# Kernel optimization log

Measured on AMD Instinct MI355X. Metric: run time of the kernel, lower is better.

## Reference

```python
import jax, jax.numpy as jnp
import numpy as np


def hadamard_matrix(n):
    # Sylvester construction; n must be a power of 2.
    H = np.array([[1.0]], dtype=np.float32)
    while H.shape[0] < n:
        H = np.block([[H, H], [H, -H]])
    return H


def setup_inputs() -> dict:
    key = jax.random.key(0)
    k1, k2, k3 = jax.random.split(key, 3)
    B, C, Hh, Ww, P = 8, 64, 256, 256, 4
    x = jax.random.normal(k1, (B, C, Hh, Ww), dtype=jnp.float32)
    v = jax.random.uniform(k2, (P, Hh, Ww), dtype=jnp.float32)          # torch.rand init
    T = jax.random.uniform(k3, (P, Hh, Ww), dtype=jnp.float32) / 10.0   # torch.rand/10 init
    return {"x": x, "v": v, "T": T}


def _wht2d(u, Hm, sc):
    # normalized Walsh-Hadamard transform along last two axes (H symmetric)
    u = jnp.einsum('...hw,vw->...hv', u, Hm) * sc   # axis=-1
    u = jnp.einsum('...hv,gh->...gv', u, Hm) * sc   # axis=-2
    return u


def reference(x, v, T):
    n = x.shape[-1]  # 256, power of 2; height_pad==height so no padding
    Hm = jnp.asarray(hadamard_matrix(n), dtype=x.dtype)
    sc = jnp.asarray(1.0 / np.sqrt(n), dtype=x.dtype)
    f2 = _wht2d(x, Hm, sc)                              # (B,C,H,W)
    a = f2[None] * v[:, None, None]                     # (P,B,C,H,W)
    st = jnp.tanh(a) * jax.nn.relu(jnp.abs(a) - jnp.abs(T)[:, None, None])
    f6 = st.sum(axis=0)                                 # (B,C,H,W)
    f8 = _wht2d(f6, Hm, sc)
    return f8 + x                                       # residual=True
```

## Files before the change

kernel.cpp:

```cpp
#include <hip/hip_runtime.h>
#include <hip/hip_fp16.h>


#define NPX 65536
#define SC  0.0625f

__device__ __forceinline__ unsigned int h2u(__half2 h) {
  union { __half2 h; unsigned int u; } c; c.h = h; return c.u;
}
__device__ __forceinline__ __half2 u2h(unsigned int u) {
  union { __half2 h; unsigned int u; } c; c.u = u; return c.h;
}

__device__ __forceinline__ void fwht16(float f[16]) {
  #pragma unroll
  for (int d = 1; d < 16; d <<= 1) {
    #pragma unroll
    for (int i = 0; i < 16; ++i) {
      if (!(i & d)) {
        float a = f[i], b = f[i | d];
        f[i]     = a + b;
        f[i | d] = a - b;
      }
    }
  }
}

__device__ __forceinline__ void fwht256_wave(float r[4], int lane) {
  float a0 = r[0] + r[1], b0 = r[0] - r[1];
  float a1 = r[2] + r[3], b1 = r[2] - r[3];
  r[0] = a0 + a1; r[1] = b0 + b1; r[2] = a0 - a1; r[3] = b0 - b1;
  #pragma unroll
  for (int m = 1; m <= 32; m <<= 1) {
    const float s = (lane & m) ? -1.0f : 1.0f;
    #pragma unroll
    for (int j = 0; j < 4; ++j) {
      float t = __shfl_xor(r[j], m);
      r[j] = fmaf(r[j], s, t);
    }
  }
}

__device__ __forceinline__ float g_term(float a, float absT) {
  float e  = __builtin_amdgcn_exp2f(a * 2.8853900817779268f);
  float th = 1.0f - 2.0f * __builtin_amdgcn_rcpf(e + 1.0f);
  float rl = fmaxf(fabsf(a) - absT, 0.0f);
  return th * rl;
}

__global__ __launch_bounds__(256) void k_prep(const float* __restrict__ v,
                                              const float* __restrict__ T,
                                              unsigned int* __restrict__ W) {
  const int i = 4 * (blockIdx.x * 256 + threadIdx.x);
  const float4 v4 = *reinterpret_cast<const float4*>(v + i);
  const float4 t4 = *reinterpret_cast<const float4*>(T + i);
  uint4 w;
  w.x = h2u(__floats2half2_rn(v4.x, fabsf(t4.x)));
  w.y = h2u(__floats2half2_rn(v4.y, fabsf(t4.y)));
  w.z = h2u(__floats2half2_rn(v4.z, fabsf(t4.z)));
  w.w = h2u(__floats2half2_rn(v4.w, fabsf(t4.w)));
  *reinterpret_cast<uint4*>(W + i) = w;
}

__global__ __launch_bounds__(1024) void k_fused(const float* __restrict__ x,
                                                const unsigned int* __restrict__ W,
                                                float* __restrict__ out) {
  __shared__ __half S[256 * 256];
  const int tid  = threadIdx.x;
  const int lane = tid & 63;
  const int wv   = tid >> 6;
  const size_t pbase = (size_t)blockIdx.x * NPX;

  #pragma unroll 2
  for (int rr = 0; rr < 16; ++rr) {
    const int row = wv * 16 + rr;
    const float4 xv = *reinterpret_cast<const float4*>(x + pbase + (size_t)row * 256 + 4 * lane);
    float r[4] = {xv.x, xv.y, xv.z, xv.w};
    fwht256_wave(r, lane);
    uint2 pk;
    pk.x = h2u(__floats2half2_rn(r[0] * SC, r[1] * SC));
    pk.y = h2u(__floats2half2_rn(r[2] * SC, r[3] * SC));
    *reinterpret_cast<uint2*>(&S[row * 256 + 4 * lane]) = pk;
  }
  __syncthreads();

  const int q = tid & 63;
  const int g = tid >> 6;
  const int c   = tid & 255;
  const int grp = tid >> 8;
  float fp[2][16];

  #pragma unroll 1
  for (int hs = 0; hs < 2; ++hs) {
    const int cb = 2 * q + 128 * hs;
    #pragma unroll
    for (int k = 0; k < 16; ++k) {
      unsigned int d = *reinterpret_cast<unsigned int*>(&S[(16 * g + k) * 256 + cb]);
      float2 e = __half22float2(u2h(d));
      fp[0][k] = e.x; fp[1][k] = e.y;
    }
    fwht16(fp[0]); fwht16(fp[1]);
    #pragma unroll
    for (int k = 0; k < 16; ++k) {
      *reinterpret_cast<unsigned int*>(&S[(16 * g + k) * 256 + cb]) =
          h2u(__floats2half2_rn(fp[0][k], fp[1][k]));
    }
  }
  __syncthreads();

  {
    float f[16];
    #pragma unroll 1
    for (int gg = grp; gg < 16; gg += 4) {
      #pragma unroll
      for (int a = 0; a < 16; ++a)
        f[a] = __half2float(S[(gg + 16 * a) * 256 + c]);
      fwht16(f);
      #pragma unroll
      for (int a = 0; a < 16; ++a) f[a] *= SC;

      #pragma unroll 4
      for (int a = 0; a < 16; ++a) {
        const int off = (gg + 16 * a) * 256 + c;
        float acc = 0.f;
        #pragma unroll
        for (int p = 0; p < 4; ++p) {
          const float2 w = __half22float2(u2h(W[p * NPX + off]));
          acc += g_term(f[a] * w.x, w.y);
        }
        f[a] = acc;
      }

      fwht16(f);
      #pragma unroll
      for (int a = 0; a < 16; ++a)
        S[(gg + 16 * a) * 256 + c] = __float2half_rn(f[a] * SC);
    }
  }
  __syncthreads();

  #pragma unroll 1
  for (int hs = 0; hs < 2; ++hs) {
    const int cb = 2 * q + 128 * hs;
    #pragma unroll
    for (int k = 0; k < 16; ++k) {
      unsigned int d = *reinterpret_cast<unsigned int*>(&S[(16 * g + k) * 256 + cb]);
      float2 e = __half22float2(u2h(d));
      fp[0][k] = e.x; fp[1][k] = e.y;
    }
    fwht16(fp[0]); fwht16(fp[1]);
    #pragma unroll
    for (int k = 0; k < 16; ++k) {
      *reinterpret_cast<unsigned int*>(&S[(16 * g + k) * 256 + cb]) =
          h2u(__floats2half2_rn(fp[0][k], fp[1][k]));
    }
  }
  __syncthreads();

  #pragma unroll 2
  for (int rr = 0; rr < 16; ++rr) {
    const int row = wv * 16 + rr;
    uint2 pk = *reinterpret_cast<uint2*>(&S[row * 256 + 4 * lane]);
    float2 lo = __half22float2(u2h(pk.x));
    float2 hi = __half22float2(u2h(pk.y));
    float r[4] = {lo.x, lo.y, hi.x, hi.y};
    fwht256_wave(r, lane);
    const float4 xv = *reinterpret_cast<const float4*>(x + pbase + (size_t)row * 256 + 4 * lane);
    float4 o;
    o.x = fmaf(r[0], SC, xv.x);
    o.y = fmaf(r[1], SC, xv.y);
    o.z = fmaf(r[2], SC, xv.z);
    o.w = fmaf(r[3], SC, xv.w);
    *reinterpret_cast<float4*>(out + pbase + (size_t)row * 256 + 4 * lane) = o;
  }
}

extern "C" void kernel_launch(void* const* d_in, const int* in_sizes, int n_in,
                              void* d_out, int out_size, void* d_ws, size_t ws_size,
                              hipStream_t stream) {
  const float* x = (const float*)d_in[0];
  const float* v = (const float*)d_in[1];
  const float* T = (const float*)d_in[2];
  float* out = (float*)d_out;
  unsigned int* W = (unsigned int*)d_ws;

  k_prep<<<256, 256, 0, stream>>>(v, T, W);
  k_fused<<<512, 1024, 0, stream>>>(x, W, out);
}
```

Measured before the change: 172.3 us.

## Replace wave-shuffle row WHT with two-pass 16x16 LDS decomposition and padded pitch

```diff
diff --git a/kernel.cpp b/kernel.cpp
--- a/kernel.cpp
+++ b/kernel.cpp
@@ -2,8 +2,9 @@
 #include <hip/hip_fp16.h>
 
 
-#define NPX 65536
-#define SC  0.0625f
+#define NPX   65536
+#define PITCH 264
+#define SC    0.0625f
 
 __device__ __forceinline__ unsigned int h2u(__half2 h) {
   union { __half2 h; unsigned int u; } c; c.h = h; return c.u;
@@ -22,21 +23,6 @@
         f[i]     = a + b;
         f[i | d] = a - b;
       }
-    }
-  }
-}
-
-__device__ __forceinline__ void fwht256_wave(float r[4], int lane) {
-  float a0 = r[0] + r[1], b0 = r[0] - r[1];
-  float a1 = r[2] + r[3], b1 = r[2] - r[3];
-  r[0] = a0 + a1; r[1] = b0 + b1; r[2] = a0 - a1; r[3] = b0 - b1;
-  #pragma unroll
-  for (int m = 1; m <= 32; m <<= 1) {
-    const float s = (lane & m) ? -1.0f : 1.0f;
-    #pragma unroll
-    for (int j = 0; j < 4; ++j) {
-      float t = __shfl_xor(r[j], m);
-      r[j] = fmaf(r[j], s, t);
     }
   }
 }
@@ -65,56 +51,85 @@
 __global__ __launch_bounds__(1024) void k_fused(const float* __restrict__ x,
                                                 const unsigned int* __restrict__ W,
                                                 float* __restrict__ out) {
-  __shared__ __half S[256 * 256];
-  const int tid  = threadIdx.x;
-  const int lane = tid & 63;
-  const int wv   = tid >> 6;
+  __shared__ __align__(16) __half S[256 * PITCH];
+  const int tid = threadIdx.x;
   const size_t pbase = (size_t)blockIdx.x * NPX;
 
-  #pragma unroll 2
-  for (int rr = 0; rr < 16; ++rr) {
-    const int row = wv * 16 + rr;
-    const float4 xv = *reinterpret_cast<const float4*>(x + pbase + (size_t)row * 256 + 4 * lane);
-    float r[4] = {xv.x, xv.y, xv.z, xv.w};
-    fwht256_wave(r, lane);
-    uint2 pk;
-    pk.x = h2u(__floats2half2_rn(r[0] * SC, r[1] * SC));
-    pk.y = h2u(__floats2half2_rn(r[2] * SC, r[3] * SC));
-    *reinterpret_cast<uint2*>(&S[row * 256 + 4 * lane]) = pk;
+  #pragma unroll 1
+  for (int it = 0; it < 4; ++it) {
+    const int task = it * 1024 + tid;
+    const int row = task >> 4, seg = task & 15;
+    const float* xp = x + pbase + (size_t)row * 256 + seg * 16;
+    float f[16];
+    #pragma unroll
+    for (int j = 0; j < 4; ++j) {
+      const float4 t4 = *reinterpret_cast<const float4*>(xp + 4 * j);
+      f[4*j] = t4.x; f[4*j+1] = t4.y; f[4*j+2] = t4.z; f[4*j+3] = t4.w;
+    }
+    fwht16(f);
+    __half* sp = &S[row * PITCH + seg * 16];
+    uint4 w0, w1;
+    w0.x = h2u(__floats2half2_rn(f[0],  f[1]));
+    w0.y = h2u(__floats2half2_rn(f[2],  f[3]));
+    w0.z = h2u(__floats2half2_rn(f[4],  f[5]));
+    w0.w = h2u(__floats2half2_rn(f[6],  f[7]));
+    w1.x = h2u(__floats2half2_rn(f[8],  f[9]));
+    w1.y = h2u(__floats2half2_rn(f[10], f[11]));
+    w1.z = h2u(__floats2half2_rn(f[12], f[13]));
+    w1.w = h2u(__floats2half2_rn(f[14], f[15]));
+    *reinterpret_cast<uint4*>(sp)     = w0;
+    *reinterpret_cast<uint4*>(sp + 8) = w1;
+  }
+  __syncthreads();
+
+  #pragma unroll 1
+  for (int it = 0; it < 2; ++it) {
+    const int task = it * 1024 + tid;
+    const int wk2 = task & 7;
+    const int row = task >> 3;
+    unsigned int* sp = reinterpret_cast<unsigned int*>(&S[row * PITCH]) + wk2;
+    float fA[16], fB[16];
+    #pragma unroll
+    for (int a = 0; a < 16; ++a) {
+      const float2 e = __half22float2(u2h(sp[8 * a]));
+      fA[a] = e.x; fB[a] = e.y;
+    }
+    fwht16(fA); fwht16(fB);
+    #pragma unroll
+    for (int a = 0; a < 16; ++a)
+      sp[8 * a] = h2u(__floats2half2_rn(fA[a] * SC, fB[a] * SC));
   }
   __syncthreads();
 
   const int q = tid & 63;
   const int g = tid >> 6;
-  const int c   = tid & 255;
-  const int grp = tid >> 8;
-  float fp[2][16];
-
   #pragma unroll 1
   for (int hs = 0; hs < 2; ++hs) {
     const int cb = 2 * q + 128 * hs;
+    float fA[16], fB[16];
     #pragma unroll
     for (int k = 0; k < 16; ++k) {
-      unsigned int d = *reinterpret_cast<unsigned int*>(&S[(16 * g + k) * 256 + cb]);
-      float2 e = __half22float2(u2h(d));
-      fp[0][k] = e.x; fp[1][k] = e.y;
-    }
-    fwht16(fp[0]); fwht16(fp[1]);
-    #pragma unroll
-    for (int k = 0; k < 16; ++k) {
-      *reinterpret_cast<unsigned int*>(&S[(16 * g + k) * 256 + cb]) =
-          h2u(__floats2half2_rn(fp[0][k], fp[1][k]));
-    }
+      const float2 e = __half22float2(
+          u2h(*reinterpret_cast<unsigned int*>(&S[(16 * g + k) * PITCH + cb])));
+      fA[k] = e.x; fB[k] = e.y;
+    }
+    fwht16(fA); fwht16(fB);
+    #pragma unroll
+    for (int k = 0; k < 16; ++k)
+      *reinterpret_cast<unsigned int*>(&S[(16 * g + k) * PITCH + cb]) =
+          h2u(__floats2half2_rn(fA[k], fB[k]));
   }
   __syncthreads();
 
   {
+    const int c   = tid & 255;
+    const int grp = tid >> 8;
     float f[16];
     #pragma unroll 1
     for (int gg = grp; gg < 16; gg += 4) {
       #pragma unroll
       for (int a = 0; a < 16; ++a)
-        f[a] = __half2float(S[(gg + 16 * a) * 256 + c]);
+        f[a] = __half2float(S[(gg + 16 * a) * PITCH + c]);
       fwht16(f);
       #pragma unroll
       for (int a = 0; a < 16; ++a) f[a] *= SC;
@@ -134,7 +149,7 @@
       fwht16(f);
       #pragma unroll
       for (int a = 0; a < 16; ++a)
-        S[(gg + 16 * a) * 256 + c] = __float2half_rn(f[a] * SC);
+        S[(gg + 16 * a) * PITCH + c] = __float2half_rn(f[a] * SC);
     }
   }
   __syncthreads();
@@ -142,36 +157,71 @@
   #pragma unroll 1
   for (int hs = 0; hs < 2; ++hs) {
     const int cb = 2 * q + 128 * hs;
+    float fA[16], fB[16];
     #pragma unroll
     for (int k = 0; k < 16; ++k) {
-      unsigned int d = *reinterpret_cast<unsigned int*>(&S[(16 * g + k) * 256 + cb]);
-      float2 e = __half22float2(u2h(d));
-      fp[0][k] = e.x; fp[1][k] = e.y;
-    }
-    fwht16(fp[0]); fwht16(fp[1]);
-    #pragma unroll
-    for (int k = 0; k < 16; ++k) {
-      *reinterpret_cast<unsigned int*>(&S[(16 * g + k) * 256 + cb]) =
-          h2u(__floats2half2_rn(fp[0][k], fp[1][k]));
-    }
-  }
-  __syncthreads();
-
-  #pragma unroll 2
-  for (int rr = 0; rr < 16; ++rr) {
-    const int row = wv * 16 + rr;
-    uint2 pk = *reinterpret_cast<uint2*>(&S[row * 256 + 4 * lane]);
-    float2 lo = __half22float2(u2h(pk.x));
-    float2 hi = __half22float2(u2h(pk.y));
-    float r[4] = {lo.x, lo.y, hi.x, hi.y};
-    fwht256_wave(r, lane);
-    const float4 xv = *reinterpret_cast<const float4*>(x + pbase + (size_t)row * 256 + 4 * lane);
-    float4 o;
-    o.x = fmaf(r[0], SC, xv.x);
-    o.y = fmaf(r[1], SC, xv.y);
-    o.z = fmaf(r[2], SC, xv.z);
-    o.w = fmaf(r[3], SC, xv.w);
-    *reinterpret_cast<float4*>(out + pbase + (size_t)row * 256 + 4 * lane) = o;
+      const float2 e = __half22float2(
+          u2h(*reinterpret_cast<unsigned int*>(&S[(16 * g + k) * PITCH + cb])));
+      fA[k] = e.x; fB[k] = e.y;
+    }
+    fwht16(fA); fwht16(fB);
+    #pragma unroll
+    for (int k = 0; k < 16; ++k)
+      *reinterpret_cast<unsigned int*>(&S[(16 * g + k) * PITCH + cb]) =
+          h2u(__floats2half2_rn(fA[k], fB[k]));
+  }
+  __syncthreads();
+
+  #pragma unroll 1
+  for (int it = 0; it < 2; ++it) {
+    const int task = it * 1024 + tid;
+    const int wk2 = task & 7;
+    const int row = task >> 3;
+    unsigned int* sp = reinterpret_cast<unsigned int*>(&S[row * PITCH]) + wk2;
+    float fA[16], fB[16];
+    #pragma unroll
+    for (int a = 0; a < 16; ++a) {
+      const float2 e = __half22float2(u2h(sp[8 * a]));
+      fA[a] = e.x; fB[a] = e.y;
+    }
+    fwht16(fA); fwht16(fB);
+    #pragma unroll
+    for (int a = 0; a < 16; ++a)
+      sp[8 * a] = h2u(__floats2half2_rn(fA[a], fB[a]));
+  }
+  __syncthreads();
+
+  #pragma unroll 1
+  for (int it = 0; it < 4; ++it) {
+    const int task = it * 1024 + tid;
+    const int row = task >> 4, seg = task & 15;
+    const __half* sp = &S[row * PITCH + seg * 16];
+    const uint4 w0 = *reinterpret_cast<const uint4*>(sp);
+    const uint4 w1 = *reinterpret_cast<const uint4*>(sp + 8);
+    float f[16];
+    { float2 e;
+      e = __half22float2(u2h(w0.x)); f[0]  = e.x; f[1]  = e.y;
+      e = __half22float2(u2h(w0.y)); f[2]  = e.x; f[3]  = e.y;
+      e = __half22float2(u2h(w0.z)); f[4]  = e.x; f[5]  = e.y;
+      e = __half22float2(u2h(w0.w)); f[6]  = e.x; f[7]  = e.y;
+      e = __half22float2(u2h(w1.x)); f[8]  = e.x; f[9]  = e.y;
+      e = __half22float2(u2h(w1.y)); f[10] = e.x; f[11] = e.y;
+      e = __half22float2(u2h(w1.z)); f[12] = e.x; f[13] = e.y;
+      e = __half22float2(u2h(w1.w)); f[14] = e.x; f[15] = e.y;
+    }
+    fwht16(f);
+    const float* xp = x + pbase + (size_t)row * 256 + seg * 16;
+    float* op = out + pbase + (size_t)row * 256 + seg * 16;
+    #pragma unroll
+    for (int j = 0; j < 4; ++j) {
+      const float4 xv = *reinterpret_cast<const float4*>(xp + 4 * j);
+      float4 o;
+      o.x = fmaf(f[4*j],     SC, xv.x);
+      o.y = fmaf(f[4*j + 1], SC, xv.y);
+      o.z = fmaf(f[4*j + 2], SC, xv.z);
+      o.w = fmaf(f[4*j + 3], SC, xv.w);
+      *reinterpret_cast<float4*>(op + 4 * j) = o;
+    }
   }
 }
 
```

After: 285.5 us. 65.7% more time.
